# Optimization experiments

Measured on AMD Instinct MI355X. Metric: run time of the kernel, lower is better.

The kernel has to match this reference:

```python
import jax, jax.numpy as jnp
import numpy as np
from math import factorial

# ---- static sizes from S2ConvNet_original ----
B_IN, B1, B2 = 30, 10, 6   # bandwidths: input S2 grid, after conv1 (SO3), after conv2 (SO3)
F1, F2, FOUT = 20, 40, 10
BATCH = 128


def _wigner_d(l, beta):
    """Wigner small-d matrix d^l_{m',m}(beta); rows m'=-l..l, cols m=-l..l."""
    cb, sb = np.cos(beta / 2.0), np.sin(beta / 2.0)
    d = np.zeros((2 * l + 1, 2 * l + 1))
    for i, mp in enumerate(range(-l, l + 1)):
        for j, m in enumerate(range(-l, l + 1)):
            pref = np.sqrt(float(factorial(l + mp) * factorial(l - mp) * factorial(l + m) * factorial(l - m)))
            acc = 0.0
            for s in range(max(0, m - mp), min(l + m, l - mp) + 1):
                den = factorial(l + m - s) * factorial(s) * factorial(mp - m + s) * factorial(l - mp - s)
                acc += ((-1.0) ** (mp - m + s) / den) * cb ** (2 * l + m - mp - 2 * s) * sb ** (mp - m + 2 * s)
            d[i, j] = pref * acc
    return d


def _dh_quad(b):
    """Driscoll-Healy beta grid / weights: sum_j w_j g(beta_j) ~ int_0^pi g(b) sin(b) db."""
    j = np.arange(2 * b)
    beta = np.pi * (2 * j + 1) / (4 * b)
    k = np.arange(b)[:, None]
    w = (2.0 / b) * np.sin(beta) * np.sum(np.sin((2 * k + 1) * beta[None, :]) / (2 * k + 1), axis=0)
    return beta, w


def _s2_grid(max_beta=np.pi / 8, n_alpha=8, n_beta=3):
    beta = np.arange(1, n_beta + 1) * max_beta / n_beta
    alpha = np.linspace(0, 2 * np.pi, n_alpha, endpoint=False)
    Bm, Am = np.meshgrid(beta, alpha, indexing='ij')
    return np.stack([Bm.ravel(), Am.ravel()], 1)  # [24, 2]


def _so3_grid(max_beta=np.pi / 8, max_gamma=2 * np.pi, n_alpha=8, n_beta=3, n_gamma=8):
    beta = np.arange(1, n_beta + 1) * max_beta / n_beta
    alpha = np.linspace(0, 2 * np.pi, n_alpha, endpoint=False)
    pre_gamma = np.linspace(0, max_gamma, n_gamma, endpoint=False)
    Bm, Am, Cm = np.meshgrid(beta, alpha, pre_gamma, indexing='ij')
    return np.stack([Bm.ravel(), Am.ravel(), (Cm - Am).ravel()], 1)  # [192, 3]


# ---------- conv1: S2 analysis (b 30 -> 10) ----------
_beta30, _qw30 = _dh_quad(B_IN)
_A1 = np.concatenate(
    [np.stack([_wigner_d(l, bb)[:, l] for bb in _beta30])  # d^l_{m,0}(beta_j): [60, 2l+1]
     * (_qw30 * (2 * np.pi / (2 * B_IN)))[:, None]
     for l in range(B1)], axis=1)  # [60, 100]
_A1J = jnp.asarray(_A1.astype(np.float32))
_M1 = np.concatenate([np.arange(-l, l + 1) for l in range(B1)])
_M1_IDX = np.mod(_M1, 2 * B_IN)

_g1 = _s2_grid()
_Y1 = np.concatenate(
    [np.stack([_wigner_d(l, bb)[:, l] for bb in _g1[:, 0]])
     * np.exp(-1j * np.outer(_g1[:, 1], np.arange(-l, l + 1)))
     for l in range(B1)], axis=1)  # [24, 100] complex
_Y1J = jnp.asarray(_Y1.astype(np.complex64))
_SC1 = float(1.0 / np.sqrt(len(_g1) * 1 * (B1 ** 4) / (B_IN ** 2)))

# ---------- SO3 synthesis tables at b=10 ----------
_beta10, _qw10 = _dh_quad(B1)
_D1S = [jnp.asarray(((2 * l + 1) * np.stack([_wigner_d(l, bb) for bb in _beta10])).astype(np.float32)) for l in range(B1)]
_FM1 = [np.mod(np.arange(-l, l + 1), 2 * B1) for l in range(B1)]

# ---------- conv2: SO3 analysis (b 10 -> 6) ----------
_W3 = np.concatenate(
    [(np.stack([_wigner_d(l, bb) for bb in _beta10])  # [20, 2l+1, 2l+1]
      * (_qw10 * (2 * np.pi / (2 * B1)) ** 2)[:, None, None]).reshape(2 * B1, -1)
     for l in range(B2)], axis=1)  # [20, 286]
_W3J = jnp.asarray(_W3.astype(np.float32))
_M2 = np.concatenate([np.repeat(np.arange(-l, l + 1), 2 * l + 1) for l in range(B2)])
_N2 = np.concatenate([np.tile(np.arange(-l, l + 1), 2 * l + 1) for l in range(B2)])
_M2_IDX = np.mod(_M2, 2 * B1)
_N2_IDX = np.mod(_N2, 2 * B1)

_g2 = _so3_grid()
_Y2 = np.concatenate(
    [np.stack([_wigner_d(l, bb) for bb in _g2[:, 0]]).reshape(len(_g2), -1)
     * (np.exp(-1j * np.outer(_g2[:, 1], np.arange(-l, l + 1)))[:, :, None]
        * np.exp(-1j * np.outer(_g2[:, 2], np.arange(-l, l + 1)))[:, None, :]).reshape(len(_g2), -1)
     for l in range(B2)], axis=1)  # [192, 286] complex: D^l_{mn}(alpha,beta,gamma)
_Y2J = jnp.asarray(_Y2.astype(np.complex64))
_SC2 = float(1.0 / np.sqrt(len(_g2) * F1 * (B2 ** 3) / (B1 ** 3)))

# ---------- SO3 synthesis tables at b=6 + integration weights ----------
_beta6, _qw6 = _dh_quad(B2)
_D2S = [jnp.asarray(((2 * l + 1) * np.stack([_wigner_d(l, bb) for bb in _beta6])).astype(np.float32)) for l in range(B2)]
_FM2 = [np.mod(np.arange(-l, l + 1), 2 * B2) for l in range(B2)]
_W_INT = jnp.asarray((_qw6 * (2 * np.pi / (2 * B2)) ** 2).astype(np.float32))


def _forward(x, k1, bias1, k2, bias2, w_out, b_lin):
    Bn = x.shape[0]
    # ===== conv1: S2 correlation -> function on SO(3) at b=10 =====
    xf = jnp.fft.fft(x.astype(jnp.complex64), axis=-1)                 # FFT over alpha: [B,1,60,60]
    xhat = jnp.einsum('bfjs,js->sbf', xf[..., _M1_IDX], _A1J)          # [100,B,1] S2 spectrum
    k1h = jnp.einsum('iop,ps->sio', (k1 * _SC1).astype(jnp.complex64), _Y1J)  # [100,1,F1]
    Ffreq = jnp.zeros((Bn, F1, 2 * B1, 2 * B1, 2 * B1), jnp.complex64)  # [B,F1,beta,m,n]
    for l in range(B1):
        s0, s1 = l * l, (l + 1) * (l + 1)
        # z^l_{mn} = sum_fin xhat^l_m conj(khat^l_n)  (outer product per degree l)
        zl = jnp.einsum('mbi,nio->bmno', xhat[s0:s1], jnp.conj(k1h[s0:s1]))
        fb = jnp.einsum('bmno,jmn->bojmn', zl, _D1S[l])                # (2l+1) d^l_{mn}(beta_j)
        Ffreq = Ffreq.at[:, :, :, _FM1[l][:, None], _FM1[l][None, :]].add(fb)
    x1 = jnp.fft.ifft2(Ffreq, axes=(-2, -1)).real * float((2 * B1) ** 2)  # synth over alpha,gamma
    x1 = jax.nn.relu(x1 + bias1[None, :, None, None, None])            # [B,F1,20,20,20]
    # ===== conv2: SO(3) correlation -> b=6 =====
    x1f = jnp.fft.fft2(x1.astype(jnp.complex64), axes=(-2, -1))        # FFT over alpha,gamma
    xhat2 = jnp.einsum('bfjs,js->sbf', x1f[:, :, :, _M2_IDX, _N2_IDX], _W3J)  # [286,B,F1]
    k2h = jnp.einsum('iop,ps->sio', (k2 * _SC2).astype(jnp.complex64), _Y2J)  # [286,F1,F2]
    Ffreq2 = jnp.zeros((Bn, F2, 2 * B2, 2 * B2, 2 * B2), jnp.complex64)
    base = 0
    for l in range(B2):
        L = 2 * l + 1
        xl = xhat2[base:base + L * L].reshape(L, L, Bn, F1)            # [m,k,B,Fin]
        gl = jnp.conj(k2h[base:base + L * L].reshape(L, L, F1, F2))    # [n,k,Fin,Fout]
        zl = jnp.einsum('mkbi,nkio->bmno', xl, gl)                     # z^l = xhat^l ghat^l^H
        fb = jnp.einsum('bmno,jmn->bojmn', zl, _D2S[l])
        Ffreq2 = Ffreq2.at[:, :, :, _FM2[l][:, None], _FM2[l][None, :]].add(fb)
        base += L * L
    x2 = jnp.fft.ifft2(Ffreq2, axes=(-2, -1)).real * float((2 * B2) ** 2)
    x2 = jax.nn.relu(x2 + bias2[None, :, None, None, None])            # [B,F2,12,12,12]
    # ===== so3_integrate + linear head =====
    feat = jnp.einsum('bfjkp,j->bf', x2, _W_INT)                       # [B,F2]
    return feat @ w_out.T + b_lin


def setup_inputs() -> dict:
    key = jax.random.key(0)
    ks = jax.random.split(key, 4)
    return {
        'x': jax.random.normal(ks[0], (BATCH, 1, 2 * B_IN, 2 * B_IN), jnp.float32),
        'k1': jax.random.normal(ks[1], (1, F1, len(_g1)), jnp.float32),
        'bias1': jnp.zeros((F1,), jnp.float32),
        'k2': jax.random.normal(ks[2], (F1, F2, len(_g2)), jnp.float32),
        'bias2': jnp.zeros((F2,), jnp.float32),
        'w_out': jax.random.normal(ks[3], (FOUT, F2), jnp.float32) / np.sqrt(F2).astype(np.float32),
        'b_lin': jnp.zeros((FOUT,), jnp.float32),
    }


def reference(x, k1, bias1, k2, bias2, w_out, b_lin):
    return _forward(x, k1, bias1, k2, bias2, w_out, b_lin)
```

## Files before the change

### kernel.cpp

```cpp
#include <hip/hip_runtime.h>
#include <math.h>

#define PI_D 3.14159265358979323846

#define BATCH 128
#define F1 20
#define F2 40
#define FOUT 10
#define NS1 100
#define NS2 286
#define NH2 146

typedef float v2f __attribute__((ext_vector_type(2)));
#define PKFMA(a,b,c) __builtin_elementwise_fma((a),(b),(c))
#define SW(v) __builtin_shufflevector((v),(v),1,0)
static __device__ __forceinline__ v2f bc2(float s){ return (v2f){s,s}; }
static __device__ __forceinline__ v2f ldv(const float2* p){ return *(const v2f*)p; }

#define GLOAD_LDS16(g,l) __builtin_amdgcn_global_load_lds( \
  (const __attribute__((address_space(1))) void*)(g), \
  (__attribute__((address_space(3))) void*)(l), 16, 0, 0)

__constant__ int ZB10c[11] = {0,1,10,35,84,165,286,455,680,969,1330};
__constant__ int B2OFFc[7] = {0,1,10,35,84,165,286};
__constant__ int HOFFc[7]  = {0,1,6,19,44,85,146};
__constant__ float2 E8c[8] = {
  { 1.f, 0.f}, { 0.70710678118654752f,-0.70710678118654752f},
  { 0.f,-1.f}, {-0.70710678118654752f,-0.70710678118654752f},
  {-1.f, 0.f}, {-0.70710678118654752f, 0.70710678118654752f},
  { 0.f, 1.f}, { 0.70710678118654752f, 0.70710678118654752f}};

#define WFENCE do{ __builtin_amdgcn_sched_barrier(0); \
  asm volatile("s_waitcnt lgkmcnt(0)" ::: "memory"); \
  __builtin_amdgcn_sched_barrier(0); }while(0)

__device__ inline void h_decode(int h, int& l, int& m, int& n){
  l=0; while(HOFFc[l+1]<=h) ++l;
  int r=h-HOFFc[l], L=2*l+1;
  if(r<l+1){ n=0; m=r; }
  else { int q=r-(l+1); n=q/L+1; m=q%L-l; }
}

__device__ inline double ipow_d(double x, int n){ double r=1.0; for(int i=0;i<n;++i) r*=x; return r; }

__device__ double wigd_t(int l, int mp, int m, double beta, const double* F){
  double cb=cos(0.5*beta), sb=sin(0.5*beta);
  double pref=sqrt(F[l+mp]*F[l-mp]*F[l+m]*F[l-m]);
  int s0 = (m-mp>0) ? (m-mp) : 0;
  int s1 = (l+m < l-mp) ? (l+m) : (l-mp);
  double acc=0.0;
  for(int s=s0;s<=s1;++s){
    double den=F[l+m-s]*F[s]*F[mp-m+s]*F[l-mp-s];
    double t=ipow_d(cb,2*l+m-mp-2*s)*ipow_d(sb,mp-m+2*s)/den;
    acc += ((mp-m+s)&1)? -t : t;
  }
  return pref*acc;
}

__device__ double dhw(int b, int j){
  double beta=PI_D*(2*j+1)/(4.0*b);
  double s=0.0;
  for(int k=0;k<b;++k) s += sin((2*k+1)*beta)/(2*k+1);
  return (2.0/b)*sin(beta)*s;
}

__global__ void gen_all(const float* __restrict__ k2,
                        float* A1, float* D1SJ, float* W3H, float* D2SJ,
                        float* D3_2, float* D3_1, float* WINT,
                        float2* E60, float2* E20, float2* E12,
                        unsigned* zLUT, unsigned* xh2LUT, unsigned* h2LUT,
                        unsigned short* fhLUT, unsigned* aLUT,
                        float2* KA){
  __shared__ double factS[21];
  __shared__ double dhwS[60];
  __shared__ float2 E8L[8];
  int blk=blockIdx.x, t=threadIdx.x;
  if(t==0){ double f=1.0; factS[0]=1.0; for(int k=1;k<=20;++k){ f*=(double)k; factS[k]=f; } }
  if(blk<24){ if(t<60) dhwS[t]=dhw(30,t); }
  else if(blk>=76 && blk<82){ if(t<20) dhwS[t]=dhw(10,t); }
  if(t<8) E8L[t]=E8c[t];
  __syncthreads();
  const double* F=factS;
  if(blk<24){
    int idx=blk*256+t;
    if(idx<6000){
      int j=idx/NS1, s=idx%NS1;
      int l=0; while((l+1)*(l+1)<=s) ++l;
      int m=s-l*l-l;
      double beta=PI_D*(2*j+1)/120.0;
      A1[idx]=(float)(wigd_t(l,m,0,beta,F)*dhwS[j]*(2.0*PI_D/60.0));
    }
  } else if(blk<76){
    int idx=(blk-24)*256+t; if(idx>=13300) return;
    int j=idx/1330, s=idx%1330;
    int l=0; while(ZB10c[l+1]<=s) ++l;
    int r=s-ZB10c[l]; int L=2*l+1;
    int mi=r/L, ni=r%L;
    double beta=PI_D*(2*j+1)/40.0;
    float v=(float)((2*l+1)*wigd_t(l,mi-l,ni-l,beta,F));
    D1SJ[j*1330+s]=v;
    int s2=ZB10c[l]+(2*l-mi)*L+ni;
    D1SJ[(19-j)*1330+s2]=(ni&1)? -v : v;
  } else if(blk<82){
    int idx=(blk-76)*256+t;
    if(idx<10*NH2){
      int j=idx/NH2, h=idx%NH2;
      int l,m,n; h_decode(h,l,m,n);
      double beta=PI_D*(2*j+1)/40.0;
      double c=2.0*PI_D/20.0;
      float v=(float)(wigd_t(l,m,n,beta,F)*dhwS[j]*c*c);
      W3H[j*NH2+h]=v;
      if(n==0){
        W3H[(19-j)*NH2+h]=((l+m)&1)? -v : v;
      } else {
        int L=2*l+1;
        int hp=HOFFc[l]+(l+1)+(n-1)*L+(l-m);
        W3H[(19-j)*NH2+hp]=((l+n)&1)? -v : v;
      }
    }
  } else if(blk<89){
    int idx=(blk-82)*256+t; if(idx>=1716) return;
    int j=idx/286, s=idx%286;
    int l=0; while(B2OFFc[l+1]<=s) ++l;
    int r=s-B2OFFc[l]; int L=2*l+1;
    int mi=r/L, ni=r%L;
    double beta=PI_D*(2*j+1)/24.0;
    float v=(float)((2*l+1)*wigd_t(l,mi-l,ni-l,beta,F));
    D2SJ[j*286+s]=v;
    int s2=B2OFFc[l]+(2*l-mi)*L+ni;
    D2SJ[(11-j)*286+s2]=(ni&1)? -v : v;
  } else if(blk<93){
    int idx=(blk-89)*256+t; if(idx>=3*286) return;
    int bi=idx/286, s=idx%286;
    int l=0; while(B2OFFc[l+1]<=s) ++l;
    int r=s-B2OFFc[l]; int L=2*l+1;
    int mi=r/L, ni=r%L;
    double beta=(bi+1)*(PI_D/8.0)/3.0;
    D3_2[idx]=(float)wigd_t(l,mi-l,ni-l,beta,F);
  } else if(blk<95){
    int idx=(blk-93)*256+t; if(idx>=3*100) return;
    int bi=idx/100, s=idx%100;
    int l=0; while((l+1)*(l+1)<=s) ++l;
    int m=s-l*l-l;
    double beta=(bi+1)*(PI_D/8.0)/3.0;
    D3_1[idx]=(float)wigd_t(l,m,0,beta,F);
  } else if(blk==95){
    if(t<12){ double c=2.0*PI_D/12.0; WINT[t]=(float)(dhw(6,t)*c*c); }
    if(t<60){ double a=2.0*PI_D*t/60.0; E60[t]=make_float2((float)cos(a),(float)sin(a)); }
    if(t<20){ double a=2.0*PI_D*t/20.0; E20[t]=make_float2((float)cos(a),(float)sin(a)); }
    if(t<12){ double a=2.0*PI_D*t/12.0; E12[t]=make_float2((float)cos(a),(float)sin(a)); }
  } else if(blk<102){
    int idx=(blk-96)*256+t; if(idx>=1330) return;
    int l=0; while(ZB10c[l+1]<=idx) ++l;
    int r=idx-ZB10c[l], L=2*l+1;
    int mi=r/L, ni=r%L;
    unsigned s1x=(unsigned)(l*l+mi), s1k=(unsigned)(l*l+ni);
    zLUT[idx]=s1x|(s1k<<16);
  } else if(blk==102){
    if(t<146){
      int l,m,n; h_decode(t,l,m,n);
      int L=2*l+1;
      int s2 =B2OFFc[l]+(m+l)*L+(n+l);
      int s2p=B2OFFc[l]+(l-m)*L+(l-n);
      unsigned sg=(unsigned)((m+n)&1);
      xh2LUT[t]=(unsigned)s2 | ((unsigned)s2p<<10) | (sg<<20);
      h2LUT[t]=(unsigned)l | ((unsigned)(m+l)<<4) | ((unsigned)(n+l)<<8) | ((unsigned)s2<<12);
      fhLUT[t]=(unsigned short)((n==0)? m : 6+(n-1)*11+(m+5));
    }
  } else if(blk==103){
    if(t==0){
      int idx=0;
      for(int lm=0;lm<10;++lm){
        for(int m=0;m<10;++m){
          int nlo=(m==0)?0:-9;
          for(int n=nlo;n<10;++n){
            int an=n<0?-n:n;
            int lmin=m>an?m:an;
            if(lmin!=lm) continue;
            int L=2*lm+1;
            int zi=ZB10c[lm]+(m+lm)*L+(n+lm);
            aLUT[idx++]=(unsigned)zi | ((unsigned)m<<11) | ((unsigned)(n+9)<<15) | ((unsigned)lm<<20);
          }
        }
      }
    }
  } else {
    int idx=(blk-104)*256+t;
    if(idx<153600){
      int ai=idx&7, q=(idx>>3)&7;
      int r2=idx>>6;
      int bi=r2%3, io=r2/3;
      const float* kp=k2+(size_t)io*192+bi*64+ai*8;
      v2f acc={0.f,0.f};
      int ph=0;
      #pragma unroll
      for(int gi=0;gi<8;++gi){
        acc=PKFMA(bc2(kp[gi]), ldv(&E8L[ph]), acc);
        ph=(ph+q)&7;
      }
      KA[(size_t)io*192+bi*64+q*8+ai]=make_float2(acc.x,acc.y);
    }
  }
}

__global__ __launch_bounds__(256) void front_k(const float* __restrict__ x,
    const float* __restrict__ k1, const float2* __restrict__ KA,
    const float* __restrict__ D3_2,
    const float2* __restrict__ E60, const float* __restrict__ A1,
    const float* __restrict__ D3_1,
    const unsigned* __restrict__ h2LUT, const unsigned* __restrict__ xh2LUT,
    float2* __restrict__ XHAT, float2* __restrict__ K1H, float2* __restrict__ K2H){
  int blk=blockIdx.x, t=threadIdx.x;
  if(blk<128){
    __shared__ __align__(16) float xs[3600];
    __shared__ float2 E60s[60];
    __shared__ float2 XFs[1140];
    if(t<60){ float2 e=E60[t]; E60s[t]=make_float2(e.x,-e.y); }
    {
      const float4* src=(const float4*)(x+blk*3600);
      float4* dst=(float4*)xs;
      for(int i=t;i<900;i+=256) GLOAD_LDS16(src+i, dst+(i&~63));
    }
    __syncthreads();
    for(int idx=t; idx<1140; idx+=256){
      int j=idx/19, mi=idx%19;
      int step=(mi<9)? mi+51 : mi-9;
      bool modd = ((mi&1)==0);
      const float* xr=xs+j*60;
      v2f acc={0.f,0.f};
      int k=0;
      for(int a=0;a<30;++a){
        float xv = modd ? (xr[a]-xr[a+30]) : (xr[a]+xr[a+30]);
        acc=PKFMA(bc2(xv), ldv(&E60s[k]), acc);
        k+=step; if(k>=60)k-=60;
      }
      XFs[idx]=make_float2(acc.x,acc.y);
    }
    __syncthreads();
    for(int s=t; s<100; s+=256){
      int l=0; while((l+1)*(l+1)<=s) ++l;
      int m=s-l*l-l;
      const float2* xf=&XFs[m+9];
      v2f acc={0.f,0.f};
      for(int j=0;j<60;++j){
        acc=PKFMA(bc2(A1[j*NS1+s]), ldv(&xf[j*19]), acc);
      }
      XHAT[blk*NS1+s]=make_float2(acc.x,acc.y);
    }
  } else if(blk<136){
    __shared__ float2 E8s[8];
    if(t<8) E8s[t]=E8c[t];
    __syncthreads();
    int idx=(blk-128)*256+t;
    if(idx<F1*NS1){
      int o=idx/NS1, s=idx%NS1;
      int l=0; while((l+1)*(l+1)<=s) ++l;
      int m=s-l*l-l;
      int mm=m&7;
      v2f acc={0.f,0.f};
      for(int bi=0;bi<3;++bi){
        v2f sum={0.f,0.f};
        int q=0;
        #pragma unroll
        for(int ai=0;ai<8;++ai){
          sum=PKFMA(bc2(k1[o*24+bi*8+ai]), ldv(&E8s[q]), sum);
          q=(q+mm)&7;
        }
        acc=PKFMA(bc2(D3_1[bi*100+s]), sum, acc);
      }
      const float SC1f = 0.06123724356957945f;
      K1H[idx]=make_float2(acc.x*SC1f, acc.y*SC1f);
    }
  } else {
    __shared__ float2 kaS[192];
    __shared__ float2 E8k[8];
    int io=blk-136;
    int i=io/F2, o=io%F2;
    if(t<8) E8k[t]=E8c[t];
    if(t<192) kaS[t]=KA[(size_t)io*192+t];
    __syncthreads();
    if(t>=146) return;
    unsigned hu=h2LUT[t];
    int l=hu&15, mi=(hu>>4)&15, ni=(hu>>8)&15, s2=hu>>12;
    int m=mi-l, n=ni-l;
    unsigned xu=xh2LUT[t];
    int s2p=(xu>>10)&1023;
    float sg=((xu>>20)&1)? -1.f : 1.f;
    int q=n&7, p=(m-n)&7;
    v2f a1={0.f,0.f}, a2=a1;
    for(int bi=0;bi<3;++bi){
      const float2* kp=&kaS[bi*64+q*8];
      v2f s1={0.f,0.f}, s2v=s1;
      int ph=0;
      #pragma unroll
      for(int ai=0;ai<8;++ai){
        v2f ka=ldv(&kp[ai]), e=ldv(&E8k[ph]);
        s1=PKFMA(ka,e,s1); s2v=PKFMA(ka,SW(e),s2v);
        ph=(ph+p)&7;
      }
      v2f dv=bc2(D3_2[bi*286+s2]);
      a1=PKFMA(dv,s1,a1); a2=PKFMA(dv,s2v,a2);
    }
    const float SC2f = 0.034722222222222224f;
    float re=(a1.x-a1.y)*SC2f, im=(a2.x+a2.y)*SC2f;
    K2H[((size_t)o*286+s2)*F1+i]=make_float2(re,im);
    K2H[((size_t)o*286+s2p)*F1+i]=make_float2(sg*re,-sg*im);
  }
}

__global__ __launch_bounds__(512,6) void fused1(
    const float2* __restrict__ XHAT, const float2* __restrict__ K1H,
    const float* __restrict__ D1SJ, const float* __restrict__ W3H,
    const float2* __restrict__ E20, const float* __restrict__ bias1,
    const unsigned* __restrict__ zLUT, const unsigned* __restrict__ xh2LUT,
    const unsigned short* __restrict__ fhLUT, const unsigned* __restrict__ aLUT,
    float2* __restrict__ XH2){
  const int b=blockIdx.x, o=blockIdx.y, t=threadIdx.x;
  const int ln=t&63, w=t>>6;
  __shared__ __align__(16) float2 zS[1330];
  __shared__ __align__(16) float2 TWE2[400];
  __shared__ __align__(16) float2 regA[8][200];
  __shared__ __align__(16) float2 regB[8][190];

  for(int idx=t; idx<400; idx+=512){
    int r=idx/20, c=idx%20;
    TWE2[idx]=E20[(r*c)%20];
  }
  {
    float2* st=regA[0];
    if(t<100) st[t]=XHAT[b*NS1+t];
    else if(t<200) st[t]=K1H[o*NS1+(t-100)];
  }
  __syncthreads();
  {
    const float2* st=regA[0];
    for(int idx=t; idx<1330; idx+=512){
      unsigned u=zLUT[idx];
      v2f xa=ldv(&st[u&0xffff]);
      v2f kb=ldv(&st[100+(u>>16)]);
      v2f p1=xa*kb, p2=xa*SW(kb);
      zS[idx]=make_float2(p1.x+p1.y, p2.y-p2.x);
    }
  }
  __syncthreads();

  const float bb1=bias1[o];
  float2* G  = regA[w];
  float*  vbF= (float*)regA[w];
  float2* Fq = regA[w];
  float*  RB = (float*)regB[w];
  float*  Sx = RB;
  float*  Sy = RB+180;
  float*  T0f= RB+360;
  float2* U_T= regB[w];
  v2f fa0={0.f,0.f}, fa1=fa0, fa2=fa0;

  const int BROW[19]={11,12,13,14,15,16,17,18,19,0,1,2,3,4,5,6,7,8,9};

  for(int jq=0;jq<3;++jq){
    const int j=jq*8+w;
    const bool act=(j<20);
    const float* Dg=D1SJ + (act? j*1330 : 0);
    if(act) for(int idx=ln; idx<181; idx+=64){
      unsigned au=aLUT[idx];
      int zi=au&2047;
      int m=(au>>11)&15, n9=(au>>15)&31, l=(au>>20)&15;
      int L=2*l+1;
      int m2=2*m+2;
      v2f a0={0.f,0.f};
      for(; l<10; ++l){
        a0=PKFMA(ldv(&zS[zi]), bc2(Dg[zi]), a0);
        zi += L*L + 2*L + m2; L += 2;
      }
      *(v2f*)&G[m*19+n9]=a0;
    }
    WFENCE;
    if(act){
    if(ln<45){
      int mb=ln/5+1, gp=(ln%5)*2;
      const float2* Gr=&G[mb*19];
      v2f E1a={0.f,0.f},E2a=E1a,O1a=E1a,O2a=E1a;
      v2f E1b=E1a,E2b=E1a,O1b=E1a,O2b=E1a;
      #pragma unroll
      for(int c=0;c<19;++c){
        v2f gv=ldv(&Gr[c]);
        const float* er=(const float*)&TWE2[BROW[c]*20+gp];
        float4 e01=*(const float4*)er;
        v2f e0={e01.x,e01.y}, e1={e01.z,e01.w};
        if(c&1){
          E1a=PKFMA(gv,e0,E1a); E2a=PKFMA(gv,SW(e0),E2a);
          E1b=PKFMA(gv,e1,E1b); E2b=PKFMA(gv,SW(e1),E2b);
        } else {
          O1a=PKFMA(gv,e0,O1a); O2a=PKFMA(gv,SW(e0),O2a);
          O1b=PKFMA(gv,e1,O1b); O2b=PKFMA(gv,SW(e1),O2b);
        }
      }
      int si=(mb-1)*20+gp;
      float exa=E1a.x-E1a.y, oxa=O1a.x-O1a.y;
      float eya=E2a.x+E2a.y, oya=O2a.x+O2a.y;
      float exb=E1b.x-E1b.y, oxb=O1b.x-O1b.y;
      float eyb=E2b.x+E2b.y, oyb=O2b.x+O2b.y;
      *(v2f*)&Sx[si]   =(v2f){2.f*(exa+oxa), 2.f*(exb+oxb)};
      *(v2f*)&Sx[si+10]=(v2f){2.f*(exa-oxa), 2.f*(exb-oxb)};
      *(v2f*)&Sy[si]   =(v2f){2.f*(eya+oya), 2.f*(eyb+oyb)};
      *(v2f*)&Sy[si+10]=(v2f){2.f*(eya-oya), 2.f*(eyb-oyb)};
    } else if(ln<50){
      int gt=(ln-45)*2;
      float g0x=G[9].x;
      float Ea=0.f,Eb=0.f,Oa=0.f,Ob=0.f;
      #pragma unroll
      for(int n=1;n<10;++n){
        float2 gv=G[9+n];
        const float* er=(const float*)&TWE2[n*20+gt];
        float4 e01=*(const float4*)er;
        float ra=gv.x*e01.x-gv.y*e01.y;
        float rb=gv.x*e01.z-gv.y*e01.w;
        if((n&1)==0){ Ea+=ra; Eb+=rb; } else { Oa+=ra; Ob+=rb; }
      }
      T0f[gt]   =g0x+2.f*(Ea+Oa);
      T0f[gt+1] =g0x+2.f*(Eb+Ob);
      T0f[gt+10]=g0x+2.f*(Ea-Oa);
      T0f[gt+11]=g0x+2.f*(Eb-Ob);
    }
    }
    WFENCE;
    if(act && ln<50){
      int a=ln/5, g0=(ln%5)*4;
      v2f i01={T0f[g0]+bb1, T0f[g0+1]+bb1};
      v2f i23={T0f[g0+2]+bb1, T0f[g0+3]+bb1};
      v2f P01={0.f,0.f},P23=P01,Q01=P01,Q23=P01;
      #pragma unroll
      for(int m=1;m<10;++m){
        float2 e=TWE2[a*20+m];
        v2f sx01=*(const v2f*)&Sx[(m-1)*20+g0];
        v2f sx23=*(const v2f*)&Sx[(m-1)*20+g0+2];
        v2f sy01=*(const v2f*)&Sy[(m-1)*20+g0];
        v2f sy23=*(const v2f*)&Sy[(m-1)*20+g0+2];
        if(m&1){
          Q01=PKFMA(bc2(e.x),sx01,Q01); Q01=PKFMA(bc2(-e.y),sy01,Q01);
          Q23=PKFMA(bc2(e.x),sx23,Q23); Q23=PKFMA(bc2(-e.y),sy23,Q23);
        } else {
          P01=PKFMA(bc2(e.x),sx01,P01); P01=PKFMA(bc2(-e.y),sy01,P01);
          P23=PKFMA(bc2(e.x),sx23,P23); P23=PKFMA(bc2(-e.y),sy23,P23);
        }
      }
      v2f z2={0.f,0.f};
      v2f vA01=i01+P01+Q01, vA23=i23+P23+Q23;
      v2f vB01=i01+P01-Q01, vB23=i23+P23-Q23;
      *(v2f*)&vbF[a*20+g0]       =__builtin_elementwise_max(vA01,z2);
      *(v2f*)&vbF[a*20+g0+2]     =__builtin_elementwise_max(vA23,z2);
      *(v2f*)&vbF[(a+10)*20+g0]  =__builtin_elementwise_max(vB01,z2);
      *(v2f*)&vbF[(a+10)*20+g0+2]=__builtin_elementwise_max(vB23,z2);
    }
    WFENCE;
    if(act && ln<60){
      int a=ln/3, np=ln%3;
      int nu0=2*np, nu1=2*np+1;
      int r0=(np==0)?0:(20-2*np);
      int r1=19-2*np;
      const float* vp=&vbF[a*20];
      const float2* T0r=&TWE2[r0*20];
      const float2* T1r=&TWE2[r1*20];
      v2f u0={0.f,0.f}, u1=u0;
      #pragma unroll
      for(int g=0;g<10;++g){
        float va=vp[g], vb=vp[g+10];
        u0=PKFMA(bc2(va+vb), ldv(&T0r[g]), u0);
        u1=PKFMA(bc2(va-vb), ldv(&T1r[g]), u1);
      }
      *(v2f*)&U_T[nu0*20+a]=u0; *(v2f*)&U_T[nu1*20+a]=u1;
    }
    WFENCE;
    if(act && ln<61){
      int mu,nu;
      if(ln<6){ mu=ln; nu=0; } else { int q=ln-6; nu=q/11+1; mu=q%11-5; }
      int mm=(mu+20)%20;
      int rm=(20-mm)%20;
      bool modd=(mm&1);
      const float2* Ur=&U_T[nu*20];
      const float2* Er=&TWE2[rm*20];
      v2f p1={0.f,0.f}, p2=p1;
      #pragma unroll
      for(int a=0;a<10;++a){
        v2f ua=ldv(&Ur[a]), ub=ldv(&Ur[a+10]);
        v2f u = modd ? (ua-ub) : (ua+ub);
        v2f e=ldv(&Er[a]);
        p1=PKFMA(u,e,p1);
        p2=PKFMA(u,SW(e),p2);
      }
      Fq[ln]=make_float2(p1.x-p1.y, p2.x+p2.y);
    }
    WFENCE;
    if(act){
      const float* W3r=W3H + j*NH2;
      fa0=PKFMA(bc2(W3r[ln]),    ldv(&Fq[fhLUT[ln]]),    fa0);
      fa1=PKFMA(bc2(W3r[64+ln]), ldv(&Fq[fhLUT[64+ln]]), fa1);
      if(ln<18) fa2=PKFMA(bc2(W3r[128+ln]), ldv(&Fq[fhLUT[128+ln]]), fa2);
    }
    WFENCE;
  }
  regB[w][ln]=make_float2(fa0.x,fa0.y);
  regB[w][64+ln]=make_float2(fa1.x,fa1.y);
  if(ln<18) regB[w][128+ln]=make_float2(fa2.x,fa2.y);
  __syncthreads();
  for(int h=t; h<146; h+=512){
    unsigned u=xh2LUT[h];
    int s2=u&1023, s2p=(u>>10)&1023;
    float sg=((u>>20)&1)? -1.f : 1.f;
    float2 a0=regB[0][h], a1=regB[1][h], a2=regB[2][h], a3=regB[3][h];
    float2 a4=regB[4][h], a5=regB[5][h], a6=regB[6][h], a7=regB[7][h];
    float2 a=make_float2(a0.x+a1.x+a2.x+a3.x+a4.x+a5.x+a6.x+a7.x,
                         a0.y+a1.y+a2.y+a3.y+a4.y+a5.y+a6.y+a7.y);
    XH2[(b*286+s2 )*F1+o]=a;
    XH2[(b*286+s2p)*F1+o]=make_float2(sg*a.x, -sg*a.y);
  }
}

__global__ __launch_bounds__(256,3) void fused2(
    const float2* __restrict__ XH2, const float2* __restrict__ K2H,
    const float* __restrict__ D2SJ, const float* __restrict__ WINT,
    const float2* __restrict__ E12, const float* __restrict__ bias2,
    const unsigned* __restrict__ h2LUT, const unsigned* __restrict__ xh2LUT,
    float* __restrict__ FEAT){
  const int b=blockIdx.x, o=blockIdx.y, t=threadIdx.x;
  const int ln=t&63, w=t>>6;
  __shared__ __align__(16) float2 Xs[2420];
  __shared__ __align__(16) float2 Ks[2420];
  __shared__ float2 zpS[584];
  float2* alias=(float2*)Xs;
  float2* TWE12=alias;
  float2* z2S  =alias+1744;
  float*  redS =(float*)Ks;

  const int gb[4]={0,84,165,286};
  const int hb[4]={0,44,85,146};
  for(int grp=0; grp<3; ++grp){
    int row0=gb[grp], rows=gb[grp+1]-row0;
    {
      int cnt4=rows*10;
      const float4* xsrc=(const float4*)(XH2+(size_t)(b*286+row0)*F1);
      const float4* ksrc=(const float4*)(K2H+(size_t)(o*286+row0)*F1);
      float4* xd=(float4*)Xs; float4* kd=(float4*)Ks;
      for(int i4=t;i4<cnt4;i4+=256){
        int wb=i4&~63;
        GLOAD_LDS16(xsrc+i4, xd+wb);
        GLOAD_LDS16(ksrc+i4, kd+wb);
      }
    }
    __syncthreads();
    int nh=hb[grp+1]-hb[grp];
    for(int idx=t; idx<4*nh; idx+=256){
      int hl=idx>>2, iq=idx&3;
      int h=hb[grp]+hl;
      unsigned hu=h2LUT[h];
      int l=hu&15, mi=(hu>>4)&15, ni=(hu>>8)&15;
      int L=2*l+1;
      int xr0=(B2OFFc[l]-row0)+mi*L;
      int kr0=(B2OFFc[l]-row0)+ni*L;
      v2f p1={0.f,0.f}, p2=p1;
      for(int k=0;k<L;++k){
        const float2* xp=Xs+(xr0+k)*F1+iq*5;
        const float2* kp=Ks+(kr0+k)*F1+iq*5;
        #pragma unroll
        for(int i=0;i<5;++i){
          v2f xa=ldv(&xp[i]), kb=ldv(&kp[i]);
          p1=PKFMA(xa,kb,p1);
          p2=PKFMA(xa,SW(kb),p2);
        }
      }
      zpS[iq*146+h]=make_float2(p1.x+p1.y, p2.y-p2.x);
    }
    __syncthreads();
  }
  for(int idx=t; idx<146; idx+=256){
    unsigned xu=xh2LUT[idx];
    int s2=xu&1023, s2p=(xu>>10)&1023;
    float sg=((xu>>20)&1)? -1.f : 1.f;
    float2 a;
    a.x=zpS[idx].x+zpS[146+idx].x+zpS[292+idx].x+zpS[438+idx].x;
    a.y=zpS[idx].y+zpS[146+idx].y+zpS[292+idx].y+zpS[438+idx].y;
    z2S[s2]=a;
    z2S[s2p]=make_float2(sg*a.x,-sg*a.y);
  }
  for(int idx=t; idx<144; idx+=256){
    int r=idx/12, c=idx%12;
    TWE12[idx]=E12[(r*c)%12];
  }
  __syncthreads();

  float2* base2=alias+144+w*400;
  float2* G2_0=base2; float2* G2_1=base2+66; float2* G2_2=base2+132;
  float*  SP=(float*)(base2+198);
  float*  S2x0=SP, *S2x1=SP+60, *S2x2=SP+120;
  float*  S2y0=SP+180, *S2y1=SP+240, *S2y2=SP+300;
  float*  T02=SP+360;
  float personal=0.f;
  const float b2v=bias2[o];
  const int j0=3*w, j1=3*w+1, j2=3*w+2;
  const float* Dg0=D2SJ + j0*286;
  const float* Dg1=D2SJ + j1*286;
  const float* Dg2=D2SJ + j2*286;
  const int BR12[11]={7,8,9,10,11,0,1,2,3,4,5};

  if(ln<61){
    int m,n;
    if(ln<6){m=0;n=ln;} else {int qq=ln-6;m=qq/11+1;n=qq%11-5;}
    int an=n<0?-n:n; int l=m>an?m:an; int L=2*l+1;
    int zi=B2OFFc[l]+(m+l)*L+(n+l); int m2=2*m+2;
    v2f a0={0.f,0.f}, a1=a0, a2=a0;
    for(;l<6;++l){
      v2f zv=ldv(&z2S[zi]);
      a0=PKFMA(zv, bc2(Dg0[zi]), a0);
      a1=PKFMA(zv, bc2(Dg1[zi]), a1);
      a2=PKFMA(zv, bc2(Dg2[zi]), a2);
      zi+=L*L+2*L+m2; L+=2;
    }
    int gi=m*11+(n+5);
    *(v2f*)&G2_0[gi]=a0; *(v2f*)&G2_1[gi]=a1; *(v2f*)&G2_2[gi]=a2;
  }
  WFENCE;
  if(ln<30){
    int m=ln/6+1, g=ln%6;
    v2f E1_0={0.f,0.f},E2_0=E1_0,O1_0=E1_0,O2_0=E1_0;
    v2f E1_1=E1_0,E2_1=E1_0,O1_1=E1_0,O2_1=E1_0;
    v2f E1_2=E1_0,E2_2=E1_0,O1_2=E1_0,O2_2=E1_0;
    #pragma unroll
    for(int c=0;c<11;++c){
      float2 ef=TWE12[BR12[c]*12+g];
      v2f e={ef.x,ef.y};
      v2f g0=ldv(&G2_0[m*11+c]), g1=ldv(&G2_1[m*11+c]), g2=ldv(&G2_2[m*11+c]);
      if(c&1){
        E1_0=PKFMA(g0,e,E1_0); E2_0=PKFMA(g0,SW(e),E2_0);
        E1_1=PKFMA(g1,e,E1_1); E2_1=PKFMA(g1,SW(e),E2_1);
        E1_2=PKFMA(g2,e,E1_2); E2_2=PKFMA(g2,SW(e),E2_2);
      } else {
        O1_0=PKFMA(g0,e,O1_0); O2_0=PKFMA(g0,SW(e),O2_0);
        O1_1=PKFMA(g1,e,O1_1); O2_1=PKFMA(g1,SW(e),O2_1);
        O1_2=PKFMA(g2,e,O1_2); O2_2=PKFMA(g2,SW(e),O2_2);
      }
    }
    int si=(m-1)*12+g;
    {
      float Ex=E1_0.x-E1_0.y, Ox=O1_0.x-O1_0.y;
      float Ey=E2_0.x+E2_0.y, Oy=O2_0.x+O2_0.y;
      S2x0[si]=2.f*(Ex+Ox); S2x0[si+6]=2.f*(Ex-Ox);
      S2y0[si]=2.f*(Ey+Oy); S2y0[si+6]=2.f*(Ey-Oy);
    }
    {
      float Ex=E1_1.x-E1_1.y, Ox=O1_1.x-O1_1.y;
      float Ey=E2_1.x+E2_1.y, Oy=O2_1.x+O2_1.y;
      S2x1[si]=2.f*(Ex+Ox); S2x1[si+6]=2.f*(Ex-Ox);
      S2y1[si]=2.f*(Ey+Oy); S2y1[si+6]=2.f*(Ey-Oy);
    }
    {
      float Ex=E1_2.x-E1_2.y, Ox=O1_2.x-O1_2.y;
      float Ey=E2_2.x+E2_2.y, Oy=O2_2.x+O2_2.y;
      S2x2[si]=2.f*(Ex+Ox); S2x2[si+6]=2.f*(Ex-Ox);
      S2y2[si]=2.f*(Ey+Oy); S2y2[si+6]=2.f*(Ey-Oy);
    }
  } else if(ln<42){
    int g=ln-30;
    float r0=G2_0[5].x, r1=G2_1[5].x, r2=G2_2[5].x;
    #pragma unroll
    for(int n=1;n<6;++n){
      float2 e=TWE12[n*12+g];
      float2 g0=G2_0[5+n], g1=G2_1[5+n], g2=G2_2[5+n];
      r0+=2.f*(g0.x*e.x-g0.y*e.y);
      r1+=2.f*(g1.x*e.x-g1.y*e.y);
      r2+=2.f*(g2.x*e.x-g2.y*e.y);
    }
    T02[g]=r0; T02[12+g]=r1; T02[24+g]=r2;
  }
  WFENCE;
  if(ln<36){
    float w0=WINT[j0], w1=WINT[j1], w2=WINT[j2];
    int a=ln/3, g4=(ln%3)*4;
    v2f iA0={T02[g4]+b2v, T02[g4+1]+b2v},       iB0={T02[g4+2]+b2v, T02[g4+3]+b2v};
    v2f iA1={T02[12+g4]+b2v, T02[12+g4+1]+b2v}, iB1={T02[12+g4+2]+b2v, T02[12+g4+3]+b2v};
    v2f iA2={T02[24+g4]+b2v, T02[24+g4+1]+b2v}, iB2={T02[24+g4+2]+b2v, T02[24+g4+3]+b2v};
    #pragma unroll
    for(int m=1;m<6;++m){
      float2 e=TWE12[a*12+m];
      v2f ex=bc2(e.x), eny=bc2(-e.y);
      int si=(m-1)*12+g4;
      v2f sx, sy;
      sx=*(const v2f*)&S2x0[si];   sy=*(const v2f*)&S2y0[si];
      iA0=PKFMA(ex,sx,iA0); iA0=PKFMA(eny,sy,iA0);
      sx=*(const v2f*)&S2x0[si+2]; sy=*(const v2f*)&S2y0[si+2];
      iB0=PKFMA(ex,sx,iB0); iB0=PKFMA(eny,sy,iB0);
      sx=*(const v2f*)&S2x1[si];   sy=*(const v2f*)&S2y1[si];
      iA1=PKFMA(ex,sx,iA1); iA1=PKFMA(eny,sy,iA1);
      sx=*(const v2f*)&S2x1[si+2]; sy=*(const v2f*)&S2y1[si+2];
      iB1=PKFMA(ex,sx,iB1); iB1=PKFMA(eny,sy,iB1);
      sx=*(const v2f*)&S2x2[si];   sy=*(const v2f*)&S2y2[si];
      iA2=PKFMA(ex,sx,iA2); iA2=PKFMA(eny,sy,iA2);
      sx=*(const v2f*)&S2x2[si+2]; sy=*(const v2f*)&S2y2[si+2];
      iB2=PKFMA(ex,sx,iB2); iB2=PKFMA(eny,sy,iB2);
    }
    v2f z2={0.f,0.f};
    v2f rA0=__builtin_elementwise_max(iA0,z2), rB0=__builtin_elementwise_max(iB0,z2);
    v2f rA1=__builtin_elementwise_max(iA1,z2), rB1=__builtin_elementwise_max(iB1,z2);
    v2f rA2=__builtin_elementwise_max(iA2,z2), rB2=__builtin_elementwise_max(iB2,z2);
    personal += w0*(rA0.x+rA0.y+rB0.x+rB0.y)
              + w1*(rA1.x+rA1.y+rB1.x+rB1.y)
              + w2*(rA2.x+rA2.y+rB2.x+rB2.y);
  }
  redS[t]=personal;
  __syncthreads();
  for(int s=128;s>0;s>>=1){
    if(t<s) redS[t]+=redS[t+s];
    __syncthreads();
  }
  if(t==0) FEAT[b*F2+o]=redS[0];
}

__global__ void head_k(const float* __restrict__ FEAT, const float* __restrict__ w_out,
                       const float* __restrict__ b_lin, float* __restrict__ out){
  int idx=blockIdx.x*blockDim.x+threadIdx.x;
  if(idx>=BATCH*FOUT) return;
  int b=idx/FOUT, q=idx%FOUT;
  float acc=b_lin[q];
  for(int f=0;f<F2;++f) acc += FEAT[b*F2+f]*w_out[q*F2+f];
  out[idx]=acc;
}

extern "C" void kernel_launch(void* const* d_in, const int* in_sizes, int n_in,
                              void* d_out, int out_size, void* d_ws, size_t ws_size,
                              hipStream_t stream) {
  const float* x    =(const float*)d_in[0];
  const float* k1   =(const float*)d_in[1];
  const float* bias1=(const float*)d_in[2];
  const float* k2   =(const float*)d_in[3];
  const float* bias2=(const float*)d_in[4];
  const float* w_out=(const float*)d_in[5];
  const float* b_lin=(const float*)d_in[6];
  float* out=(float*)d_out;

  char* ws=(char*)d_ws;
  float*  A1   =(float* )(ws+0);
  float*  D1SJ =(float* )(ws+24000);
  float*  W3H  =(float* )(ws+130400);
  float*  D2SJ =(float* )(ws+142080);
  float*  D3_2 =(float* )(ws+155808);
  float*  D3_1 =(float* )(ws+159248);
  float*  WINT =(float* )(ws+160448);
  float2* E60  =(float2*)(ws+160496);
  float2* E20  =(float2*)(ws+160976);
  float2* E12  =(float2*)(ws+161136);
  unsigned* zLUT=(unsigned*)(ws+161248);
  unsigned* xh2LUT=(unsigned*)(ws+166576);
  unsigned* h2LUT =(unsigned*)(ws+167160);
  unsigned short* fhLUT=(unsigned short*)(ws+167744);
  unsigned* aLUT =(unsigned*)(ws+168048);
  float2* XHAT =(float2*)(ws+168784);
  float2* K1H  =(float2*)(ws+271184);
  float2* KA   =(float2*)(ws+287184);
  float2* XH2  =(float2*)(ws+1515984);
  float2* K2H  =(float2*)(ws+7373264);
  float*  FEAT =(float* )(ws+9203664);

  (void)in_sizes; (void)n_in; (void)out_size; (void)ws_size;

  gen_all<<<704,256,0,stream>>>(k2,A1,D1SJ,W3H,D2SJ,D3_2,D3_1,WINT,E60,E20,E12,
                                zLUT,xh2LUT,h2LUT,fhLUT,aLUT,KA);
  front_k<<<936,256,0,stream>>>(x,k1,KA,D3_2,E60,A1,D3_1,h2LUT,xh2LUT,XHAT,K1H,K2H);
  dim3 g1(BATCH,F1);
  fused1<<<g1,512,0,stream>>>(XHAT,K1H,D1SJ,W3H,E20,bias1,zLUT,xh2LUT,fhLUT,aLUT,XH2);
  dim3 g2(BATCH,F2);
  fused2<<<g2,256,0,stream>>>(XH2,K2H,D2SJ,WINT,E12,bias2,h2LUT,xh2LUT,FEAT);
  head_k<<<(BATCH*FOUT+255)/256,256,0,stream>>>(FEAT,w_out,b_lin,out);
}
```

Before: 198.2 us.

## Use 10 waves in fused1 to cover 20 beta rows; halve Wigner table generation

fused1 now launches 640 threads (10 waves), so its 20 beta slices are processed in two full passes instead of three passes with idle waves. This removes the 'act' guards and the wasted third iteration, at the cost of more LDS per block and different occupancy. Separately, gen_all computes Wigner-d entries only over a triangle and fills the transposed entries through the symmetry d_{n,m} = (-1)^{m-n} d_{m,n}, which roughly halves the double-precision Wigner evaluations.

```diff
diff --git a/kernel.cpp b/kernel.cpp
--- a/kernel.cpp
+++ b/kernel.cpp
@@ -39,6 +39,13 @@
   int r=h-HOFFc[l], L=2*l+1;
   if(r<l+1){ n=0; m=r; }
   else { int q=r-(l+1); n=q/L+1; m=q%L-l; }
+}
+
+__device__ inline void tri_decode(int r, int& mi, int& ni){
+  mi=(int)((sqrtf(8.f*(float)r+1.f)-1.f)*0.5f);
+  while((mi+1)*(mi+2)/2<=r) ++mi;
+  while(mi*(mi+1)/2>r) --mi;
+  ni=r-mi*(mi+1)/2;
 }
 
 __device__ inline double ipow_d(double x, int n){ double r=1.0; for(int i=0;i<n;++i) r*=x; return r; }
@@ -91,16 +98,20 @@
       A1[idx]=(float)(wigd_t(l,m,0,beta,F)*dhwS[j]*(2.0*PI_D/60.0));
     }
   } else if(blk<76){
-    int idx=(blk-24)*256+t; if(idx>=13300) return;
-    int j=idx/1330, s=idx%1330;
-    int l=0; while(ZB10c[l+1]<=s) ++l;
-    int r=s-ZB10c[l]; int L=2*l+1;
-    int mi=r/L, ni=r%L;
+    int idx=(blk-24)*256+t; if(idx>=7150) return;
+    int j=idx/715, p=idx%715;
+    const int TRI[11]={0,1,7,22,50,95,161,252,372,525,715};
+    int l=0; while(TRI[l+1]<=p) ++l;
+    int r=p-TRI[l]; int L=2*l+1;
+    int mi,ni; tri_decode(r,mi,ni);
     double beta=PI_D*(2*j+1)/40.0;
     float v=(float)((2*l+1)*wigd_t(l,mi-l,ni-l,beta,F));
-    D1SJ[j*1330+s]=v;
-    int s2=ZB10c[l]+(2*l-mi)*L+ni;
-    D1SJ[(19-j)*1330+s2]=(ni&1)? -v : v;
+    int base=ZB10c[l];
+    float vt=((mi-ni)&1)? -v : v;
+    D1SJ[j*1330+base+mi*L+ni]=v;
+    D1SJ[j*1330+base+ni*L+mi]=vt;
+    D1SJ[(19-j)*1330+base+(2*l-mi)*L+ni]=(ni&1)? -v : v;
+    D1SJ[(19-j)*1330+base+(2*l-ni)*L+mi]=(mi&1)? -vt : vt;
   } else if(blk<82){
     int idx=(blk-76)*256+t;
     if(idx<10*NH2){
@@ -119,24 +130,32 @@
       }
     }
   } else if(blk<89){
-    int idx=(blk-82)*256+t; if(idx>=1716) return;
-    int j=idx/286, s=idx%286;
-    int l=0; while(B2OFFc[l+1]<=s) ++l;
-    int r=s-B2OFFc[l]; int L=2*l+1;
-    int mi=r/L, ni=r%L;
+    int idx=(blk-82)*256+t; if(idx>=966) return;
+    int j=idx/161, p=idx%161;
+    const int TRI2[7]={0,1,7,22,50,95,161};
+    int l=0; while(TRI2[l+1]<=p) ++l;
+    int r=p-TRI2[l]; int L=2*l+1;
+    int mi,ni; tri_decode(r,mi,ni);
     double beta=PI_D*(2*j+1)/24.0;
     float v=(float)((2*l+1)*wigd_t(l,mi-l,ni-l,beta,F));
-    D2SJ[j*286+s]=v;
-    int s2=B2OFFc[l]+(2*l-mi)*L+ni;
-    D2SJ[(11-j)*286+s2]=(ni&1)? -v : v;
+    int base=B2OFFc[l];
+    float vt=((mi-ni)&1)? -v : v;
+    D2SJ[j*286+base+mi*L+ni]=v;
+    D2SJ[j*286+base+ni*L+mi]=vt;
+    D2SJ[(11-j)*286+base+(2*l-mi)*L+ni]=(ni&1)? -v : v;
+    D2SJ[(11-j)*286+base+(2*l-ni)*L+mi]=(mi&1)? -vt : vt;
   } else if(blk<93){
-    int idx=(blk-89)*256+t; if(idx>=3*286) return;
-    int bi=idx/286, s=idx%286;
-    int l=0; while(B2OFFc[l+1]<=s) ++l;
-    int r=s-B2OFFc[l]; int L=2*l+1;
-    int mi=r/L, ni=r%L;
+    int idx=(blk-89)*256+t; if(idx>=483) return;
+    int bi=idx/161, p=idx%161;
+    const int TRI2[7]={0,1,7,22,50,95,161};
+    int l=0; while(TRI2[l+1]<=p) ++l;
+    int r=p-TRI2[l]; int L=2*l+1;
+    int mi,ni; tri_decode(r,mi,ni);
     double beta=(bi+1)*(PI_D/8.0)/3.0;
-    D3_2[idx]=(float)wigd_t(l,mi-l,ni-l,beta,F);
+    float v=(float)wigd_t(l,mi-l,ni-l,beta,F);
+    int base=B2OFFc[l];
+    D3_2[bi*286+base+mi*L+ni]=v;
+    D3_2[bi*286+base+ni*L+mi]=((mi-ni)&1)? -v : v;
   } else if(blk<95){
     int idx=(blk-93)*256+t; if(idx>=3*100) return;
     int bi=idx/100, s=idx%100;
@@ -308,7 +327,7 @@
   }
 }
 
-__global__ __launch_bounds__(512,6) void fused1(
+__global__ __launch_bounds__(640,7) void fused1(
     const float2* __restrict__ XHAT, const float2* __restrict__ K1H,
     const float* __restrict__ D1SJ, const float* __restrict__ W3H,
     const float2* __restrict__ E20, const float* __restrict__ bias1,
@@ -319,10 +338,10 @@
   const int ln=t&63, w=t>>6;
   __shared__ __align__(16) float2 zS[1330];
   __shared__ __align__(16) float2 TWE2[400];
-  __shared__ __align__(16) float2 regA[8][200];
-  __shared__ __align__(16) float2 regB[8][190];
-
-  for(int idx=t; idx<400; idx+=512){
+  __shared__ __align__(16) float2 regA[10][200];
+  __shared__ __align__(16) float2 regB[10][190];
+
+  for(int idx=t; idx<400; idx+=640){
     int r=idx/20, c=idx%20;
     TWE2[idx]=E20[(r*c)%20];
   }
@@ -334,7 +353,7 @@
   __syncthreads();
   {
     const float2* st=regA[0];
-    for(int idx=t; idx<1330; idx+=512){
+    for(int idx=t; idx<1330; idx+=640){
       unsigned u=zLUT[idx];
       v2f xa=ldv(&st[u&0xffff]);
       v2f kb=ldv(&st[100+(u>>16)]);
@@ -357,11 +376,10 @@
 
   const int BROW[19]={11,12,13,14,15,16,17,18,19,0,1,2,3,4,5,6,7,8,9};
 
-  for(int jq=0;jq<3;++jq){
-    const int j=jq*8+w;
-    const bool act=(j<20);
-    const float* Dg=D1SJ + (act? j*1330 : 0);
-    if(act) for(int idx=ln; idx<181; idx+=64){
+  for(int jq=0;jq<2;++jq){
+    const int j=jq*10+w;
+    const float* Dg=D1SJ + j*1330;
+    for(int idx=ln; idx<181; idx+=64){
       unsigned au=aLUT[idx];
       int zi=au&2047;
       int m=(au>>11)&15, n9=(au>>15)&31, l=(au>>20)&15;
@@ -375,7 +393,6 @@
       *(v2f*)&G[m*19+n9]=a0;
     }
     WFENCE;
-    if(act){
     if(ln<45){
       int mb=ln/5+1, gp=(ln%5)*2;
       const float2* Gr=&G[mb*19];
@@ -422,9 +439,8 @@
       T0f[gt+10]=g0x+2.f*(Ea-Oa);
       T0f[gt+11]=g0x+2.f*(Eb-Ob);
     }
-    }
     WFENCE;
-    if(act && ln<50){
+    if(ln<50){
       int a=ln/5, g0=(ln%5)*4;
       v2f i01={T0f[g0]+bb1, T0f[g0+1]+bb1};
       v2f i23={T0f[g0+2]+bb1, T0f[g0+3]+bb1};
@@ -453,7 +469,7 @@
       *(v2f*)&vbF[(a+10)*20+g0+2]=__builtin_elementwise_max(vB23,z2);
     }
     WFENCE;
-    if(act && ln<60){
+    if(ln<60){
       int a=ln/3, np=ln%3;
       int nu0=2*np, nu1=2*np+1;
       int r0=(np==0)?0:(20-2*np);
@@ -471,7 +487,7 @@
       *(v2f*)&U_T[nu0*20+a]=u0; *(v2f*)&U_T[nu1*20+a]=u1;
     }
     WFENCE;
-    if(act && ln<61){
+    if(ln<61){
       int mu,nu;
       if(ln<6){ mu=ln; nu=0; } else { int q=ln-6; nu=q/11+1; mu=q%11-5; }
       int mm=(mu+20)%20;
@@ -491,7 +507,7 @@
       Fq[ln]=make_float2(p1.x-p1.y, p2.x+p2.y);
     }
     WFENCE;
-    if(act){
+    {
       const float* W3r=W3H + j*NH2;
       fa0=PKFMA(bc2(W3r[ln]),    ldv(&Fq[fhLUT[ln]]),    fa0);
       fa1=PKFMA(bc2(W3r[64+ln]), ldv(&Fq[fhLUT[64+ln]]), fa1);
@@ -503,16 +519,16 @@
   regB[w][64+ln]=make_float2(fa1.x,fa1.y);
   if(ln<18) regB[w][128+ln]=make_float2(fa2.x,fa2.y);
   __syncthreads();
-  for(int h=t; h<146; h+=512){
+  if(t<146){
+    int h=t;
     unsigned u=xh2LUT[h];
     int s2=u&1023, s2p=(u>>10)&1023;
     float sg=((u>>20)&1)? -1.f : 1.f;
-    float2 a0=regB[0][h], a1=regB[1][h], a2=regB[2][h], a3=regB[3][h];
-    float2 a4=regB[4][h], a5=regB[5][h], a6=regB[6][h], a7=regB[7][h];
-    float2 a=make_float2(a0.x+a1.x+a2.x+a3.x+a4.x+a5.x+a6.x+a7.x,
-                         a0.y+a1.y+a2.y+a3.y+a4.y+a5.y+a6.y+a7.y);
-    XH2[(b*286+s2 )*F1+o]=a;
-    XH2[(b*286+s2p)*F1+o]=make_float2(sg*a.x, -sg*a.y);
+    float ax=0.f, ay=0.f;
+    #pragma unroll
+    for(int ww=0;ww<10;++ww){ float2 av=regB[ww][h]; ax+=av.x; ay+=av.y; }
+    XH2[(b*286+s2 )*F1+o]=make_float2(ax,ay);
+    XH2[(b*286+s2p)*F1+o]=make_float2(sg*ax, -sg*ay);
   }
 }
 
@@ -765,7 +781,7 @@
                                 zLUT,xh2LUT,h2LUT,fhLUT,aLUT,KA);
   front_k<<<936,256,0,stream>>>(x,k1,KA,D3_2,E60,A1,D3_1,h2LUT,xh2LUT,XHAT,K1H,K2H);
   dim3 g1(BATCH,F1);
-  fused1<<<g1,512,0,stream>>>(XHAT,K1H,D1SJ,W3H,E20,bias1,zLUT,xh2LUT,fhLUT,aLUT,XH2);
+  fused1<<<g1,640,0,stream>>>(XHAT,K1H,D1SJ,W3H,E20,bias1,zLUT,xh2LUT,fhLUT,aLUT,XH2);
   dim3 g2(BATCH,F2);
   fused2<<<g2,256,0,stream>>>(XH2,K2H,D2SJ,WINT,E12,bias2,h2LUT,xh2LUT,FEAT);
   head_k<<<(BATCH*FOUT+255)/256,256,0,stream>>>(FEAT,w_out,b_lin,out);
```

Measured after the change: 235.7 us. 1.19x slower.
